# Kernel optimization log

Hardware: AMD Instinct MI355X
Metric: run time of the kernel (lower is better)

The kernel has to match this reference:

```python
import jax, jax.numpy as jnp
import numpy as np

PRECISION = 2.0 ** 24  # ctx._precision stand-in; factor = sqrt(precision)
SF_CONST = 48.0


def setup_inputs() -> dict:
    key = jax.random.key(0)
    k1, k2, k3 = jax.random.split(key, 3)
    x = jax.random.normal(k1, (16, 128, 128, 128), dtype=jnp.float32)  # NCHW
    W = jax.random.normal(k2, (256, 128, 3, 3), dtype=jnp.float32) * 0.05  # OIHW
    b = jax.random.normal(k3, (256,), dtype=jnp.float32) * 0.1
    return {"x": x, "W": W, "b": b}


def reference(x, W, b):
    # --- quantize() (standard, non-mixture path) ---
    N = float(np.prod(W.shape[1:]))           # in_ch * kh * kw = 1152
    factor = np.sqrt(PRECISION)               # sqrt(ctx._precision)
    sf = np.sqrt(SF_CONST / N)
    w_sum = jnp.sum(jnp.abs(W), axis=(1, 2, 3))          # [O]
    w_sum = jnp.where(w_sum == 0, 1.0, w_sum)
    fw = (factor / sf - np.sqrt(N / 12.0) * 5.0) / w_sum  # [O]
    Wq = jnp.round(W * fw[:, None, None, None])

    # --- forward int-quantized conv ---
    x_max = jnp.max(jnp.abs(x))
    fx = jnp.where(x_max > 0, (factor * sf - 0.5) / x_max, 1.0)
    xq = jnp.round(fx * x)
    y = jax.lax.conv_general_dilated(
        xq, Wq,
        window_strides=(1, 1),
        padding=((1, 1), (1, 1)),
        dimension_numbers=("NCHW", "OIHW", "NCHW"),
    )
    # dequantize per output channel, then fused float bias add
    y = y / (fx * fw[:, None, None]) + b[:, None, None]
    # Activation (ReLU); BN disabled, dropout disabled in this config
    return jax.nn.relu(y)
```

## Files before the change

### kernel.cpp

```cpp
#include <hip/hip_runtime.h>
#include <math.h>


#define FW_NUM 20017.23017802413f
#define FX_NUM 835.5924988699913f
#define WQA_OFF 2048
#define WQB_OFF (640 * 1024)
#define XQ_OFF  (2 * 1024 * 1024)
#define XQ_BYTES 67108864ull

#define CK  16
#define CKP 24
#define JW  130

typedef _Float16 half8 __attribute__((ext_vector_type(8)));
typedef _Float16 half4 __attribute__((ext_vector_type(4)));
typedef float floatx16 __attribute__((ext_vector_type(16)));

__device__ __forceinline__ void gl_lds16(const void* g, void* s) {
    __builtin_amdgcn_global_load_lds((const __attribute__((address_space(1))) void*)g,
                                     (__attribute__((address_space(3))) void*)s, 16, 0, 0);
}

__global__ void xmax_kernel(const float* __restrict__ x, unsigned int* wsu, int n4) {
    int tid = blockIdx.x * blockDim.x + threadIdx.x;
    int stride = gridDim.x * blockDim.x;
    const float4* x4 = (const float4*)x;
    float m = 0.f;
    for (int i = tid; i < n4; i += stride) {
        float4 v = x4[i];
        m = fmaxf(m, fmaxf(fmaxf(fabsf(v.x), fabsf(v.y)), fmaxf(fabsf(v.z), fabsf(v.w))));
    }
    #pragma unroll
    for (int off = 32; off >= 1; off >>= 1)
        m = fmaxf(m, __shfl_down(m, off, 64));
    __shared__ float sm[4];
    if ((threadIdx.x & 63) == 0) sm[threadIdx.x >> 6] = m;
    __syncthreads();
    if (threadIdx.x == 0) {
        m = fmaxf(fmaxf(sm[0], sm[1]), fmaxf(sm[2], sm[3]));
        atomicMax(wsu, __float_as_uint(m));
    }
}

__global__ void wq_kernel(const float* __restrict__ W, float* wsf, int big) {
    int o = blockIdx.x;
    int t = threadIdx.x;
    const float* wrow = W + o * 1152;
    float wv[9];
    float s = 0.f;
    #pragma unroll
    for (int k = 0; k < 9; k++) { wv[k] = wrow[t * 9 + k]; s += fabsf(wv[k]); }
    #pragma unroll
    for (int off = 32; off >= 1; off >>= 1) s += __shfl_down(s, off, 64);
    __shared__ float sred[2];
    __shared__ float sfw;
    if ((t & 63) == 0) sred[t >> 6] = s;
    __syncthreads();
    if (t == 0) {
        float wsum = sred[0] + sred[1];
        if (wsum == 0.f) wsum = 1.f;
        float fw = FW_NUM / wsum;
        wsf[64 + o] = fw;
        sfw = fw;
    }
    __syncthreads();
    float fw = sfw;
    _Float16* wqa = (_Float16*)((char*)wsf + WQA_OFF);
    _Float16* wqb = (_Float16*)((char*)wsf + WQB_OFF);
    #pragma unroll
    for (int k = 0; k < 9; k++) {
        _Float16 hv = (_Float16)rintf(wv[k] * fw);
        wqa[(o * 9 + k) * 128 + t] = hv;
        if (big)
            wqb[(((t >> 4) * 9 + k) * 256 + o) * 16 + (t & 15)] = hv;
    }
}

__global__ void quantx_kernel(const float* __restrict__ x, const float* __restrict__ wsf,
                              _Float16* __restrict__ xq) {
    int bid = blockIdx.x;
    int h  = bid & 127;
    int cc = (bid >> 7) & 7;
    int n  = bid >> 10;
    float xmax = __uint_as_float(((const unsigned int*)wsf)[0]);
    float fx = xmax > 0.f ? FX_NUM / xmax : 1.0f;
    int w = threadIdx.x;
    const float* xp = x + ((size_t)(n * 128 + cc * 16) * 128 + h) * 128 + w;
    half8 v0, v1;
    #pragma unroll
    for (int ci = 0; ci < 8; ci++)  v0[ci] = (_Float16)rintf(fx * xp[(size_t)ci * 16384]);
    #pragma unroll
    for (int ci = 8; ci < 16; ci++) v1[ci - 8] = (_Float16)rintf(fx * xp[(size_t)ci * 16384]);
    _Float16* op = xq + ((size_t)bid * 128 + w) * 16;
    *(half8*)op = v0;
    *(half8*)(op + 8) = v1;
}

__global__ __launch_bounds__(256, 2) void conv_main(const _Float16* __restrict__ xq,
                                                    const float* __restrict__ bias,
                                                    const float* __restrict__ wsf,
                                                    float* __restrict__ out) {
    __shared__ __align__(16) _Float16 xs[2][10 * 66 * 16];
    __shared__ __align__(16) _Float16 wl[2][9 * 64 * 16];
    __shared__ float sc[64], bz[64];

    float xmax = __uint_as_float(((const unsigned int*)wsf)[0]);
    float fx = xmax > 0.f ? FX_NUM / xmax : 1.0f;

    int bx = blockIdx.x;
    int o0 = (bx & 3) << 6;
    int w0 = ((bx >> 2) & 1) << 6;
    int h0 = ((bx >> 3) & 15) << 3;
    int n  = bx >> 7;

    int tid = threadIdx.x;
    int lane = tid & 63;
    int wv = tid >> 6;
    int m32 = lane & 31;
    int q2 = lane >> 5;

    const char* wqb = (const char*)wsf + WQB_OFF;

    {
        uint4 z = {0u, 0u, 0u, 0u};
        uint4* p = (uint4*)xs;
        for (int i = tid; i < (int)(sizeof(xs) / 16); i += 256) p[i] = z;
        if (tid < 64) {
            float fwv = wsf[64 + o0 + tid];
            sc[tid] = 1.0f / (fx * fwv);
            bz[tid] = bias[o0 + tid];
        }
    }
    __syncthreads();

    floatx16 acc[2][4];
    #pragma unroll
    for (int a1 = 0; a1 < 2; a1++)
        #pragma unroll
        for (int a2 = 0; a2 < 4; a2++)
            #pragma unroll
            for (int e = 0; e < 16; e++) acc[a1][a2][e] = 0.f;

    auto stage_async = [&](int ccs, int tb) {
        for (int s = wv; s < 38; s += 4) {
            if (s < 20) {
                int r = s >> 1, hseg = s & 1;
                int h = h0 + r - 1;
                if (h >= 0 && h < 128) {
                    size_t pix = ((size_t)((n * 8 + ccs) * 128 + h)) * 128 + w0;
                    const char* src = (const char*)xq + pix * 32 + hseg * 1024 + (size_t)lane * 16;
                    char* dst = (char*)&xs[tb][(r * 66 + 1) * 16] + hseg * 1024;
                    gl_lds16(src, dst);
                }
            } else {
                int t2 = s - 20, tap = t2 >> 1, g = t2 & 1;
                const char* src = wqb + ((size_t)(ccs * 9 + tap) * 256 + o0) * 32 + g * 1024 + (size_t)lane * 16;
                char* dst = (char*)&wl[tb][tap * 64 * 16] + g * 1024;
                gl_lds16(src, dst);
            }
        }
    };
    auto halo_load = [&](int ccs) -> half8 {
        half8 v = {};
        if (tid < 40) {
            int r = tid >> 2, sd = (tid >> 1) & 1, g = tid & 1;
            int h = h0 + r - 1;
            int wh = sd ? (w0 + 64) : (w0 - 1);
            if (h >= 0 && h < 128 && wh >= 0 && wh < 128)
                v = *(const half8*)(xq + (((size_t)((n * 8 + ccs) * 128 + h)) * 128 + wh) * 16 + g * 8);
        }
        return v;
    };
    auto halo_store = [&](int tb, half8 v) {
        if (tid < 40) {
            int r = tid >> 2, sd = (tid >> 1) & 1, g = tid & 1;
            int h = h0 + r - 1;
            int wh = sd ? (w0 + 64) : (w0 - 1);
            if (h >= 0 && h < 128 && wh >= 0 && wh < 128)
                *(half8*)&xs[tb][(r * 66 + (sd ? 65 : 0)) * 16 + g * 8] = v;
        }
    };

    {
        half8 hv = halo_load(0);
        stage_async(0, 0);
        halo_store(0, hv);
    }
    __syncthreads();

    for (int cc = 0; cc < 8; ++cc) {
        int cb = cc & 1;
        half8 hn = {};
        if (cc < 7) {
            hn = halo_load(cc + 1);
            stage_async(cc + 1, cb ^ 1);
        }

        #pragma unroll
        for (int kh = 0; kh < 3; ++kh) {
            #pragma unroll
            for (int kw = 0; kw < 3; ++kw) {
                int tap = kh * 3 + kw;
                const _Float16* wp = &wl[cb][(tap * 64 + m32) * 16 + q2 * 8];
                half8 wf0 = *(const half8*)wp;
                half8 wf1 = *(const half8*)(wp + 32 * 16);
                #pragma unroll
                for (int pt = 0; pt < 4; ++pt) {
                    const _Float16* xp =
                        &xs[cb][(((wv * 2 + (pt >> 1) + kh) * 66) + (pt & 1) * 32 + m32 + kw) * 16 + q2 * 8];
                    half8 xf = *(const half8*)xp;
                    acc[0][pt] = __builtin_amdgcn_mfma_f32_32x32x16_f16(wf0, xf, acc[0][pt], 0, 0, 0);
                    acc[1][pt] = __builtin_amdgcn_mfma_f32_32x32x16_f16(wf1, xf, acc[1][pt], 0, 0, 0);
                }
            }
        }

        if (cc < 7) halo_store(cb ^ 1, hn);
        __syncthreads();
    }

    #pragma unroll
    for (int ot = 0; ot < 2; ++ot) {
        #pragma unroll
        for (int e = 0; e < 16; ++e) {
            int o_loc = ot * 32 + (e & 3) + 8 * (e >> 2) + 4 * q2;
            float scale = sc[o_loc];
            float bv = bz[o_loc];
            #pragma unroll
            for (int pt = 0; pt < 4; ++pt) {
                int h = h0 + wv * 2 + (pt >> 1);
                int w = w0 + (pt & 1) * 32 + m32;
                float v = fmaxf(fmaf(acc[ot][pt][e], scale, bv), 0.f);
                out[(((size_t)(n * 256 + o0 + o_loc)) * 128 + h) * 128 + w] = v;
            }
        }
    }
}

__global__ __launch_bounds__(256, 2) void conv_fallback(const float* __restrict__ x,
                                                        const float* __restrict__ bias,
                                                        const float* __restrict__ wsf,
                                                        float* __restrict__ out) {
    __shared__ __align__(16) _Float16 xs[6 * JW * CKP];
    __shared__ __align__(16) _Float16 wlds[9 * 64 * CKP];

    const unsigned int* wsu = (const unsigned int*)wsf;
    float xmax = __uint_as_float(wsu[0]);
    float fx = xmax > 0.f ? FX_NUM / xmax : 1.0f;

    int bx = blockIdx.x;
    int n  = bx >> 5;
    int h0 = (bx & 31) << 2;
    int o0 = blockIdx.y << 6;

    int tid  = threadIdx.x;
    int lane = tid & 63;
    int wave = tid >> 6;
    int m32  = lane & 31;
    int q2   = lane >> 5;

    const _Float16* wq16 = (const _Float16*)((const char*)wsf + WQA_OFF);
    const float* xn = x + (size_t)n * (128 * 128 * 128);

    floatx16 acc[4][2];
    #pragma unroll
    for (int mt = 0; mt < 4; mt++)
        #pragma unroll
        for (int nt = 0; nt < 2; nt++)
            #pragma unroll
            for (int e = 0; e < 16; e++) acc[mt][nt][e] = 0.f;

    if (tid < 192) {
        int r = tid >> 5;
        int s = tid & 31;
        int c = s & 15;
        int j = (s >> 4) ? (JW - 1) : 0;
        xs[(r * JW + j) * CKP + c] = (_Float16)0.f;
    }

    for (int c0 = 0; c0 < 128; c0 += CK) {
        __syncthreads();
        #pragma unroll
        for (int it = 0; it < 12; ++it) {
            int idx = tid + it * 256;
            int j  = (idx & 127) + 1;
            int c4 = (idx >> 7) & 3;
            int r  = idx >> 9;
            int h  = h0 + r - 1;
            float v0 = 0.f, v1 = 0.f, v2 = 0.f, v3 = 0.f;
            if (h >= 0 && h < 128) {
                const float* xp = xn + (size_t)(c0 + c4 * 4) * 16384 + h * 128 + (j - 1);
                v0 = xp[0]; v1 = xp[16384]; v2 = xp[32768]; v3 = xp[49152];
            }
            half4 hv;
            hv[0] = (_Float16)rintf(fx * v0);
            hv[1] = (_Float16)rintf(fx * v1);
            hv[2] = (_Float16)rintf(fx * v2);
            hv[3] = (_Float16)rintf(fx * v3);
            *(half4*)&xs[(r * JW + j) * CKP + c4 * 4] = hv;
        }
        #pragma unroll
        for (int it = 0; it < 5; ++it) {
            int idx = tid + it * 256;
            if (idx < 1152) {
                int o   = idx / 18;
                int rem = idx - o * 18;
                int tap = rem >> 1;
                int g   = rem & 1;
                half8 v = *(const half8*)(wq16 + ((size_t)(o0 + o) * 9 + tap) * 128 + c0 + g * 8);
                *(half8*)&wlds[(tap * 64 + o) * CKP + g * 8] = v;
            }
        }
        __syncthreads();

        const _Float16* xbase = &xs[(wave * JW + m32) * CKP + q2 * 8];
        const _Float16* wbase = &wlds[m32 * CKP + q2 * 8];
        #pragma unroll
        for (int kh = 0; kh < 3; ++kh) {
            #pragma unroll
            for (int kw = 0; kw < 3; ++kw) {
                int tap = kh * 3 + kw;
                half8 b0 = *(const half8*)(wbase + (tap * 64 +  0) * CKP);
                half8 b1 = *(const half8*)(wbase + (tap * 64 + 32) * CKP);
                #pragma unroll
                for (int mt = 0; mt < 4; ++mt) {
                    half8 a = *(const half8*)(xbase + (kh * JW + kw + mt * 32) * CKP);
                    acc[mt][0] = __builtin_amdgcn_mfma_f32_32x32x16_f16(a, b0, acc[mt][0], 0, 0, 0);
                    acc[mt][1] = __builtin_amdgcn_mfma_f32_32x32x16_f16(a, b1, acc[mt][1], 0, 0, 0);
                }
            }
        }
    }

    int h = h0 + wave;
    #pragma unroll
    for (int nt = 0; nt < 2; ++nt) {
        int o = o0 + nt * 32 + m32;
        float fwv = wsf[64 + o];
        float scale = 1.0f / (fx * fwv);
        float bv = bias[o];
        float* op = out + (((size_t)n * 256 + o) * 128 + h) * 128;
        #pragma unroll
        for (int mt = 0; mt < 4; ++mt) {
            #pragma unroll
            for (int g = 0; g < 4; ++g) {
                int w = mt * 32 + 8 * g + 4 * q2;
                float4 r;
                r.x = fmaxf(fmaf(acc[mt][nt][4 * g + 0], scale, bv), 0.f);
                r.y = fmaxf(fmaf(acc[mt][nt][4 * g + 1], scale, bv), 0.f);
                r.z = fmaxf(fmaf(acc[mt][nt][4 * g + 2], scale, bv), 0.f);
                r.w = fmaxf(fmaf(acc[mt][nt][4 * g + 3], scale, bv), 0.f);
                *(float4*)(op + w) = r;
            }
        }
    }
}

extern "C" void kernel_launch(void* const* d_in, const int* in_sizes, int n_in,
                              void* d_out, int out_size, void* d_ws, size_t ws_size,
                              hipStream_t stream) {
    const float* x = (const float*)d_in[0];
    const float* W = (const float*)d_in[1];
    const float* b = (const float*)d_in[2];
    float* out = (float*)d_out;
    float* wsf = (float*)d_ws;

    int big = (ws_size >= (size_t)XQ_OFF + XQ_BYTES) ? 1 : 0;

    hipMemsetAsync(d_ws, 0, 256, stream);

    xmax_kernel<<<1024, 256, 0, stream>>>(x, (unsigned int*)d_ws, (16 * 128 * 128 * 128) / 4);
    wq_kernel<<<256, 128, 0, stream>>>(W, wsf, big);

    if (big) {
        _Float16* xq = (_Float16*)((char*)d_ws + XQ_OFF);
        quantx_kernel<<<16 * 8 * 128, 128, 0, stream>>>(x, wsf, xq);
        conv_main<<<2048, 256, 0, stream>>>(xq, b, wsf, out);
    } else {
        dim3 grid(512, 4);
        conv_fallback<<<grid, 256, 0, stream>>>(x, b, wsf, out);
    }
}
```

Before: 505.0 us.

## Retile conv to 4x128 pixel by 128 channel blocks with 8-channel K chunks

```diff
diff --git a/kernel.cpp b/kernel.cpp
--- a/kernel.cpp
+++ b/kernel.cpp
@@ -68,12 +68,14 @@
     float fw = sfw;
     _Float16* wqa = (_Float16*)((char*)wsf + WQA_OFF);
     _Float16* wqb = (_Float16*)((char*)wsf + WQB_OFF);
+    int ci = t >> 3, ce = t & 7;
+    int oh = o >> 7, oi = o & 127;
     #pragma unroll
     for (int k = 0; k < 9; k++) {
         _Float16 hv = (_Float16)rintf(wv[k] * fw);
         wqa[(o * 9 + k) * 128 + t] = hv;
         if (big)
-            wqb[(((t >> 4) * 9 + k) * 256 + o) * 16 + (t & 15)] = hv;
+            wqb[((((size_t)ci * 2 + oh) * 9 + k) * 128 + oi) * 8 + ce] = hv;
     }
 }
 
@@ -81,38 +83,33 @@
                               _Float16* __restrict__ xq) {
     int bid = blockIdx.x;
     int h  = bid & 127;
-    int cc = (bid >> 7) & 7;
-    int n  = bid >> 10;
+    int ci = (bid >> 7) & 15;
+    int n  = bid >> 11;
     float xmax = __uint_as_float(((const unsigned int*)wsf)[0]);
     float fx = xmax > 0.f ? FX_NUM / xmax : 1.0f;
     int w = threadIdx.x;
-    const float* xp = x + ((size_t)(n * 128 + cc * 16) * 128 + h) * 128 + w;
-    half8 v0, v1;
-    #pragma unroll
-    for (int ci = 0; ci < 8; ci++)  v0[ci] = (_Float16)rintf(fx * xp[(size_t)ci * 16384]);
-    #pragma unroll
-    for (int ci = 8; ci < 16; ci++) v1[ci - 8] = (_Float16)rintf(fx * xp[(size_t)ci * 16384]);
-    _Float16* op = xq + ((size_t)bid * 128 + w) * 16;
-    *(half8*)op = v0;
-    *(half8*)(op + 8) = v1;
-}
-
-__global__ __launch_bounds__(256, 2) void conv_main(const _Float16* __restrict__ xq,
+    const float* xp = x + ((size_t)(n * 128 + ci * 8) * 128 + h) * 128 + w;
+    half8 v;
+    #pragma unroll
+    for (int k = 0; k < 8; k++) v[k] = (_Float16)rintf(fx * xp[(size_t)k * 16384]);
+    *(half8*)(xq + ((size_t)bid * 128 + w) * 8) = v;
+}
+
+__global__ __launch_bounds__(256, 1) void conv_main(const _Float16* __restrict__ xq,
                                                     const float* __restrict__ bias,
                                                     const float* __restrict__ wsf,
                                                     float* __restrict__ out) {
-    __shared__ __align__(16) _Float16 xs[2][10 * 66 * 16];
-    __shared__ __align__(16) _Float16 wl[2][9 * 64 * 16];
-    __shared__ float sc[64], bz[64];
+    __shared__ __align__(16) _Float16 xs[2][6 * 130 * 8];
+    __shared__ __align__(16) _Float16 wl[2][9 * 128 * 8];
 
     float xmax = __uint_as_float(((const unsigned int*)wsf)[0]);
     float fx = xmax > 0.f ? FX_NUM / xmax : 1.0f;
 
     int bx = blockIdx.x;
-    int o0 = (bx & 3) << 6;
-    int w0 = ((bx >> 2) & 1) << 6;
-    int h0 = ((bx >> 3) & 15) << 3;
-    int n  = bx >> 7;
+    int oh = bx & 1;
+    int h0 = ((bx >> 1) & 31) << 2;
+    int n  = bx >> 6;
+    int o0 = oh << 7;
 
     int tid = threadIdx.x;
     int lane = tid & 63;
@@ -121,119 +118,100 @@
     int q2 = lane >> 5;
 
     const char* wqb = (const char*)wsf + WQB_OFF;
+    const char* xbase_g = (const char*)xq + ((size_t)n * 16) * 128 * 2048;
 
     {
         uint4 z = {0u, 0u, 0u, 0u};
         uint4* p = (uint4*)xs;
+        #pragma unroll 2
         for (int i = tid; i < (int)(sizeof(xs) / 16); i += 256) p[i] = z;
-        if (tid < 64) {
-            float fwv = wsf[64 + o0 + tid];
-            sc[tid] = 1.0f / (fx * fwv);
-            bz[tid] = bias[o0 + tid];
-        }
-    }
-    __syncthreads();
-
-    floatx16 acc[2][4];
-    #pragma unroll
-    for (int a1 = 0; a1 < 2; a1++)
+    }
+    __syncthreads();
+
+    floatx16 acc[4][4];
+    #pragma unroll
+    for (int a1 = 0; a1 < 4; a1++)
         #pragma unroll
         for (int a2 = 0; a2 < 4; a2++)
             #pragma unroll
             for (int e = 0; e < 16; e++) acc[a1][a2][e] = 0.f;
 
-    auto stage_async = [&](int ccs, int tb) {
-        for (int s = wv; s < 38; s += 4) {
-            if (s < 20) {
-                int r = s >> 1, hseg = s & 1;
+    auto stage_async = [&](int ci, int tb) {
+        const char* xci = xbase_g + (size_t)ci * 128 * 2048;
+        for (int s = wv; s < 30; s += 4) {
+            if (s < 12) {
+                int r = s >> 1, seg = s & 1;
                 int h = h0 + r - 1;
                 if (h >= 0 && h < 128) {
-                    size_t pix = ((size_t)((n * 8 + ccs) * 128 + h)) * 128 + w0;
-                    const char* src = (const char*)xq + pix * 32 + hseg * 1024 + (size_t)lane * 16;
-                    char* dst = (char*)&xs[tb][(r * 66 + 1) * 16] + hseg * 1024;
+                    const char* src = xci + (size_t)h * 2048 + seg * 1024 + (size_t)lane * 16;
+                    char* dst = (char*)&xs[tb][(r * 130 + 1) * 8] + seg * 1024;
                     gl_lds16(src, dst);
                 }
             } else {
-                int t2 = s - 20, tap = t2 >> 1, g = t2 & 1;
-                const char* src = wqb + ((size_t)(ccs * 9 + tap) * 256 + o0) * 32 + g * 1024 + (size_t)lane * 16;
-                char* dst = (char*)&wl[tb][tap * 64 * 16] + g * 1024;
+                int t2 = s - 12;
+                const char* src = wqb + ((size_t)ci * 2 + oh) * 18432 + t2 * 1024 + (size_t)lane * 16;
+                char* dst = (char*)&wl[tb][0] + t2 * 1024;
                 gl_lds16(src, dst);
             }
         }
     };
-    auto halo_load = [&](int ccs) -> half8 {
-        half8 v = {};
-        if (tid < 40) {
-            int r = tid >> 2, sd = (tid >> 1) & 1, g = tid & 1;
-            int h = h0 + r - 1;
-            int wh = sd ? (w0 + 64) : (w0 - 1);
-            if (h >= 0 && h < 128 && wh >= 0 && wh < 128)
-                v = *(const half8*)(xq + (((size_t)((n * 8 + ccs) * 128 + h)) * 128 + wh) * 16 + g * 8);
-        }
-        return v;
-    };
-    auto halo_store = [&](int tb, half8 v) {
-        if (tid < 40) {
-            int r = tid >> 2, sd = (tid >> 1) & 1, g = tid & 1;
-            int h = h0 + r - 1;
-            int wh = sd ? (w0 + 64) : (w0 - 1);
-            if (h >= 0 && h < 128 && wh >= 0 && wh < 128)
-                *(half8*)&xs[tb][(r * 66 + (sd ? 65 : 0)) * 16 + g * 8] = v;
-        }
-    };
-
-    {
-        half8 hv = halo_load(0);
-        stage_async(0, 0);
-        halo_store(0, hv);
-    }
-    __syncthreads();
-
-    for (int cc = 0; cc < 8; ++cc) {
-        int cb = cc & 1;
-        half8 hn = {};
-        if (cc < 7) {
-            hn = halo_load(cc + 1);
-            stage_async(cc + 1, cb ^ 1);
-        }
-
-        #pragma unroll
-        for (int kh = 0; kh < 3; ++kh) {
-            #pragma unroll
-            for (int kw = 0; kw < 3; ++kw) {
-                int tap = kh * 3 + kw;
-                const _Float16* wp = &wl[cb][(tap * 64 + m32) * 16 + q2 * 8];
-                half8 wf0 = *(const half8*)wp;
-                half8 wf1 = *(const half8*)(wp + 32 * 16);
+
+    stage_async(0, 0);
+    __syncthreads();
+
+    for (int ci = 0; ci < 16; ++ci) {
+        int cb = ci & 1;
+        if (ci < 15) stage_async(ci + 1, cb ^ 1);
+
+        const _Float16* xb = &xs[cb][(wv * 130 + m32) * 8];
+        const _Float16* wb = &wl[cb][m32 * 8];
+
+        #pragma unroll
+        for (int p = 0; p < 5; ++p) {
+            const int t0 = 2 * p;
+            const int t1 = (2 * p + 1 > 8) ? 8 : 2 * p + 1;
+            const int x0 = ((t0 / 3) * 130 + (t0 % 3)) * 8;
+            const int x1 = ((t1 / 3) * 130 + (t1 % 3)) * 8;
+            const int w0o = t0 * 1024;
+            const int w1o = t1 * 1024;
+            int xoff = q2 ? x1 : x0;
+            int woff = q2 ? w1o : w0o;
+
+            half8 af[4], bf[4];
+            #pragma unroll
+            for (int ot = 0; ot < 4; ++ot) af[ot] = *(const half8*)(wb + woff + ot * 256);
+            if (p == 4) {
+                half8 zz = {};
+                if (q2) {
+                    #pragma unroll
+                    for (int ot = 0; ot < 4; ++ot) af[ot] = zz;
+                }
+            }
+            #pragma unroll
+            for (int pt = 0; pt < 4; ++pt) bf[pt] = *(const half8*)(xb + xoff + pt * 256);
+
+            #pragma unroll
+            for (int ot = 0; ot < 4; ++ot)
                 #pragma unroll
-                for (int pt = 0; pt < 4; ++pt) {
-                    const _Float16* xp =
-                        &xs[cb][(((wv * 2 + (pt >> 1) + kh) * 66) + (pt & 1) * 32 + m32 + kw) * 16 + q2 * 8];
-                    half8 xf = *(const half8*)xp;
-                    acc[0][pt] = __builtin_amdgcn_mfma_f32_32x32x16_f16(wf0, xf, acc[0][pt], 0, 0, 0);
-                    acc[1][pt] = __builtin_amdgcn_mfma_f32_32x32x16_f16(wf1, xf, acc[1][pt], 0, 0, 0);
-                }
-            }
-        }
-
-        if (cc < 7) halo_store(cb ^ 1, hn);
+                for (int pt = 0; pt < 4; ++pt)
+                    acc[ot][pt] = __builtin_amdgcn_mfma_f32_32x32x16_f16(af[ot], bf[pt], acc[ot][pt], 0, 0, 0);
+        }
         __syncthreads();
     }
 
-    #pragma unroll
-    for (int ot = 0; ot < 2; ++ot) {
+    int h = h0 + wv;
+    #pragma unroll
+    for (int ot = 0; ot < 4; ++ot) {
         #pragma unroll
         for (int e = 0; e < 16; ++e) {
             int o_loc = ot * 32 + (e & 3) + 8 * (e >> 2) + 4 * q2;
-            float scale = sc[o_loc];
-            float bv = bz[o_loc];
-            #pragma unroll
-            for (int pt = 0; pt < 4; ++pt) {
-                int h = h0 + wv * 2 + (pt >> 1);
-                int w = w0 + (pt & 1) * 32 + m32;
-                float v = fmaxf(fmaf(acc[ot][pt][e], scale, bv), 0.f);
-                out[(((size_t)(n * 256 + o0 + o_loc)) * 128 + h) * 128 + w] = v;
-            }
+            int o = o0 + o_loc;
+            float scale = 1.0f / (fx * wsf[64 + o]);
+            float bv = bias[o];
+            float* op = out + (((size_t)(n * 256 + o)) * 128 + h) * 128 + m32;
+            #pragma unroll
+            for (int pt = 0; pt < 4; ++pt)
+                op[pt * 32] = fmaxf(fmaf(acc[ot][pt][e], scale, bv), 0.f);
         }
     }
 }
@@ -242,7 +220,7 @@
                                                         const float* __restrict__ bias,
                                                         const float* __restrict__ wsf,
                                                         float* __restrict__ out) {
-    __shared__ __align__(16) _Float16 xs[6 * JW * CKP];
+    __shared__ __align__(16) _Float16 xsf[6 * JW * CKP];
     __shared__ __align__(16) _Float16 wlds[9 * 64 * CKP];
 
     const unsigned int* wsu = (const unsigned int*)wsf;
@@ -276,7 +254,7 @@
         int s = tid & 31;
         int c = s & 15;
         int j = (s >> 4) ? (JW - 1) : 0;
-        xs[(r * JW + j) * CKP + c] = (_Float16)0.f;
+        xsf[(r * JW + j) * CKP + c] = (_Float16)0.f;
     }
 
     for (int c0 = 0; c0 < 128; c0 += CK) {
@@ -298,7 +276,7 @@
             hv[1] = (_Float16)rintf(fx * v1);
             hv[2] = (_Float16)rintf(fx * v2);
             hv[3] = (_Float16)rintf(fx * v3);
-            *(half4*)&xs[(r * JW + j) * CKP + c4 * 4] = hv;
+            *(half4*)&xsf[(r * JW + j) * CKP + c4 * 4] = hv;
         }
         #pragma unroll
         for (int it = 0; it < 5; ++it) {
@@ -314,7 +292,7 @@
         }
         __syncthreads();
 
-        const _Float16* xbase = &xs[(wave * JW + m32) * CKP + q2 * 8];
+        const _Float16* xbase = &xsf[(wave * JW + m32) * CKP + q2 * 8];
         const _Float16* wbase = &wlds[m32 * CKP + q2 * 8];
         #pragma unroll
         for (int kh = 0; kh < 3; ++kh) {
@@ -375,10 +353,10 @@
 
     if (big) {
         _Float16* xq = (_Float16*)((char*)d_ws + XQ_OFF);
-        quantx_kernel<<<16 * 8 * 128, 128, 0, stream>>>(x, wsf, xq);
-        conv_main<<<2048, 256, 0, stream>>>(xq, b, wsf, out);
+        quantx_kernel<<<16 * 16 * 128, 128, 0, stream>>>(x, wsf, xq);
+        conv_main<<<1024, 256, 0, stream>>>(xq, b, wsf, out);
     } else {
         dim3 grid(512, 4);
-        conv_fallback<<<grid, 256, 0, stream>>>(x, b, wsf, out);
-    }
-}
+        conv_fallback<<<grid, 4 * 64, 0, stream>>>(x, b, wsf, out);
+    }
+}
```

Result: slower. 589.2 us (+16.7%).
